# Optimization experiments

Hardware: AMD Instinct MI355X
Metric: run time of the kernel (lower is better)

Reference implementation:

```python
import jax, jax.numpy as jnp
import numpy as np

T = 16384       # video length (frames)
C = 7           # out_features = d_model = num surgical phases
F_DIM = 2048    # mstcn_f_dim (spatial feature dim)
LEN_Q = 30      # sliding window length
N_HEADS = 4
D_K = 64        # attn_dim = min(64, mstcn_f_maps=64)
D_FF = 64       # d_ff = mstcn_f_maps


def setup_inputs() -> dict:
    key = jax.random.key(0)
    ks = jax.random.split(key, 10)
    w = lambda i, shape: jax.random.normal(ks[i], shape, jnp.float32) * 0.05
    return {
        "x": jax.random.normal(ks[0], (1, C, T), jnp.float32),
        "long_feature": jax.random.normal(ks[1], (1, T, F_DIM), jnp.float32),
        "W_fc": w(2, (C, F_DIM)),              # nn.Linear(mstcn_f_dim, out_features, bias=False)
        "W_q": w(3, (N_HEADS * D_K, C)),
        "W_k": w(4, (N_HEADS * D_K, C)),
        "W_v": w(5, (N_HEADS * D_K, C)),
        "W_o": w(6, (C, N_HEADS * D_K)),
        "ln1_g": jnp.ones((C,), jnp.float32),
        "ln1_b": jnp.zeros((C,), jnp.float32),
        "W_ff1": w(7, (D_FF, C)),
        "W_ff2": w(8, (C, D_FF)),
        "ln2_g": jnp.ones((C,), jnp.float32),
        "ln2_b": jnp.zeros((C,), jnp.float32),
    }


def layer_norm(x, g, b, eps=1e-5):
    mu = x.mean(-1, keepdims=True)
    var = ((x - mu) ** 2).mean(-1, keepdims=True)
    return (x - mu) * jax.lax.rsqrt(var + eps) * g + b


def reference(x, long_feature, W_fc, W_q, W_k, W_v, W_o, ln1_g, ln1_b, W_ff1, W_ff2, ln2_g, ln2_b):
    # --- vectorized sliding-window (replaces the Python loop of zeros/cat/stack) ---
    feats = x[0].T                                            # (T, C)
    padded = jnp.concatenate([jnp.zeros((LEN_Q - 1, C), feats.dtype), feats], axis=0)
    idx = jnp.arange(T)[:, None] + jnp.arange(LEN_Q)[None, :]  # window ends at frame i
    inputs = padded[idx]                                       # (T, LEN_Q, C)

    # --- spatial embedding: feas = tanh(fc(long_feature)).transpose(0,1) ---
    feas = jnp.tanh(long_feature[0] @ W_fc.T)[:, None, :]      # (T, 1, C)

    # --- decoder layer: cross MHA(query=feas, kv=inputs) + residual + LN ---
    q = (feas @ W_q.T).reshape(T, 1, N_HEADS, D_K).transpose(0, 2, 1, 3)       # (T,H,1,Dk)
    k = (inputs @ W_k.T).reshape(T, LEN_Q, N_HEADS, D_K).transpose(0, 2, 1, 3)  # (T,H,Lq,Dk)
    v = (inputs @ W_v.T).reshape(T, LEN_Q, N_HEADS, D_K).transpose(0, 2, 1, 3)  # (T,H,Lq,Dk)
    scores = jnp.einsum('thqd,thkd->thqk', q, k) / np.float32(np.sqrt(D_K))
    attn = jax.nn.softmax(scores, axis=-1)
    ctx = jnp.einsum('thqk,thkd->thqd', attn, v)
    ctx = ctx.transpose(0, 2, 1, 3).reshape(T, 1, N_HEADS * D_K)
    out = layer_norm(ctx @ W_o.T + feas, ln1_g, ln1_b)         # (T, 1, C)

    # --- position-wise FFN + residual + LN ---
    ff = jax.nn.relu(out @ W_ff1.T) @ W_ff2.T
    out = layer_norm(ff + out, ln2_g, ln2_b)
    return out[:, 0]                                           # (T, C) per-frame logits
```

## Files before the change

kernel.cpp:

```cpp
#include <hip/hip_runtime.h>
#include <math.h>

#define T_FRAMES 16384
#define FDIM 2048
#define LQ 30
#define FPB 16

__global__ __launch_bounds__(448) void setup_kernel(
    const float* __restrict__ Wq, const float* __restrict__ Wk,
    const float* __restrict__ Wv, const float* __restrict__ Wo,
    float* __restrict__ AM) {
  const int e = threadIdx.x;
  if (e >= 392) return;
  const int which = e / 196;
  const int r = e % 196;
  const int h = r / 49;
  const int rr = r % 49;
  const int c = rr / 7;
  const int c2 = rr % 7;
  float s = 0.0f;
  if (which == 0) {
    for (int d = 0; d < 64; ++d)
      s = fmaf(Wq[(h * 64 + d) * 7 + c], Wk[(h * 64 + d) * 7 + c2], s);
  } else {
    for (int d = 0; d < 64; ++d)
      s = fmaf(Wo[c * 256 + h * 64 + d], Wv[(h * 64 + d) * 7 + c2], s);
  }
  AM[e] = s;
}

__global__ __launch_bounds__(256) void fused_kernel(
    const float* __restrict__ lf,
    const float* __restrict__ Wfc,
    const float* __restrict__ x,
    const float* __restrict__ AM,
    const float* __restrict__ W1,
    const float* __restrict__ W2,
    const float* __restrict__ ln1g, const float* __restrict__ ln1b,
    const float* __restrict__ ln2g, const float* __restrict__ ln2b,
    float* __restrict__ out) {
  __shared__ float feas_s[FPB][7];
  __shared__ float AM_s[392];
  __shared__ float ft[(FPB + LQ - 1) * 7];
  __shared__ float hpart[FPB][4][7];

  const int tid = threadIdx.x;
  const int lane = tid & 63;
  const int wave = tid >> 6;
  const int t0 = blockIdx.x * FPB;

  for (int i = tid; i < 392; i += 256) AM_s[i] = AM[i];
  for (int i = tid; i < (FPB + LQ - 1) * 7; i += 256) {
    const int row = i / 7, c = i % 7;
    const int s = t0 - (LQ - 1) + row;
    ft[i] = (s >= 0) ? x[c * T_FRAMES + s] : 0.0f;
  }

  const int tf = t0 + wave * 4;
  const float* lfp = lf + (size_t)tf * FDIM;
  float acc[4][7];
#pragma unroll
  for (int fr = 0; fr < 4; ++fr)
#pragma unroll
    for (int c = 0; c < 7; ++c) acc[fr][c] = 0.0f;

  for (int chunk = 0; chunk < 8; ++chunk) {
    const int f = chunk * 256 + lane * 4;
    const float4 a0 = *(const float4*)(lfp + 0 * FDIM + f);
    const float4 a1 = *(const float4*)(lfp + 1 * FDIM + f);
    const float4 a2 = *(const float4*)(lfp + 2 * FDIM + f);
    const float4 a3 = *(const float4*)(lfp + 3 * FDIM + f);
#pragma unroll
    for (int c = 0; c < 7; ++c) {
      const float4 w = *(const float4*)(Wfc + c * FDIM + f);
      acc[0][c] = fmaf(a0.x, w.x, fmaf(a0.y, w.y, fmaf(a0.z, w.z, fmaf(a0.w, w.w, acc[0][c]))));
      acc[1][c] = fmaf(a1.x, w.x, fmaf(a1.y, w.y, fmaf(a1.z, w.z, fmaf(a1.w, w.w, acc[1][c]))));
      acc[2][c] = fmaf(a2.x, w.x, fmaf(a2.y, w.y, fmaf(a2.z, w.z, fmaf(a2.w, w.w, acc[2][c]))));
      acc[3][c] = fmaf(a3.x, w.x, fmaf(a3.y, w.y, fmaf(a3.z, w.z, fmaf(a3.w, w.w, acc[3][c]))));
    }
  }

#pragma unroll
  for (int fr = 0; fr < 4; ++fr) {
#pragma unroll
    for (int c = 0; c < 7; ++c) {
      float v = acc[fr][c];
      for (int off = 32; off > 0; off >>= 1) v += __shfl_down(v, off, 64);
      if (lane == 0) feas_s[wave * 4 + fr][c] = tanhf(v);
    }
  }
  __syncthreads();

  if (tid < FPB * 4) {
    const int f = tid >> 2;
    const int h = tid & 3;
    float fe[7];
#pragma unroll
    for (int c = 0; c < 7; ++c) fe[c] = feas_s[f][c];

    const float* Ah = AM_s + h * 49;
    const float* Mh = AM_s + 196 + h * 49;
    float qk[7];
#pragma unroll
    for (int c2 = 0; c2 < 7; ++c2) {
      float s = 0.0f;
#pragma unroll
      for (int c = 0; c < 7; ++c) s = fmaf(fe[c], Ah[c * 7 + c2], s);
      qk[c2] = s * 0.125f;
    }
    const float* frow = &ft[f * 7];
    float sc[LQ];
    float m = -1e30f;
#pragma unroll
    for (int j = 0; j < LQ; ++j) {
      const float* r = frow + j * 7;
      float s = 0.0f;
#pragma unroll
      for (int c2 = 0; c2 < 7; ++c2) s = fmaf(qk[c2], r[c2], s);
      sc[j] = s;
      m = fmaxf(m, s);
    }
    float sum = 0.0f;
    float wsum[7] = {0, 0, 0, 0, 0, 0, 0};
#pragma unroll
    for (int j = 0; j < LQ; ++j) {
      const float p = __expf(sc[j] - m);
      sum += p;
      const float* r = frow + j * 7;
#pragma unroll
      for (int c2 = 0; c2 < 7; ++c2) wsum[c2] = fmaf(p, r[c2], wsum[c2]);
    }
    const float inv = 1.0f / sum;
#pragma unroll
    for (int c = 0; c < 7; ++c) {
      float s = 0.0f;
#pragma unroll
      for (int c2 = 0; c2 < 7; ++c2) s = fmaf(Mh[c * 7 + c2], wsum[c2], s);
      hpart[f][h][c] = s * inv;
    }
  }
  __syncthreads();

  if (tid < FPB) {
    const int f = tid;
    float v[7];
#pragma unroll
    for (int c = 0; c < 7; ++c)
      v[c] = feas_s[f][c] + hpart[f][0][c] + hpart[f][1][c] + hpart[f][2][c] + hpart[f][3][c];

    float mu = 0.0f;
#pragma unroll
    for (int c = 0; c < 7; ++c) mu += v[c];
    mu *= (1.0f / 7.0f);
    float var = 0.0f;
#pragma unroll
    for (int c = 0; c < 7; ++c) { const float d = v[c] - mu; var = fmaf(d, d, var); }
    var *= (1.0f / 7.0f);
    float rs = rsqrtf(var + 1e-5f);
    float o1[7];
#pragma unroll
    for (int c = 0; c < 7; ++c) o1[c] = (v[c] - mu) * rs * ln1g[c] + ln1b[c];

    float ff[7] = {0, 0, 0, 0, 0, 0, 0};
    for (int k = 0; k < 64; ++k) {
      float hk = 0.0f;
#pragma unroll
      for (int c = 0; c < 7; ++c) hk = fmaf(W1[k * 7 + c], o1[c], hk);
      hk = fmaxf(hk, 0.0f);
#pragma unroll
      for (int c = 0; c < 7; ++c) ff[c] = fmaf(W2[c * 64 + k], hk, ff[c]);
    }

#pragma unroll
    for (int c = 0; c < 7; ++c) v[c] = ff[c] + o1[c];
    mu = 0.0f;
#pragma unroll
    for (int c = 0; c < 7; ++c) mu += v[c];
    mu *= (1.0f / 7.0f);
    var = 0.0f;
#pragma unroll
    for (int c = 0; c < 7; ++c) { const float d = v[c] - mu; var = fmaf(d, d, var); }
    var *= (1.0f / 7.0f);
    rs = rsqrtf(var + 1e-5f);
    const int t = t0 + f;
#pragma unroll
    for (int c = 0; c < 7; ++c)
      out[(size_t)t * 7 + c] = (v[c] - mu) * rs * ln2g[c] + ln2b[c];
  }
}

extern "C" void kernel_launch(void* const* d_in, const int* in_sizes, int n_in,
                              void* d_out, int out_size, void* d_ws, size_t ws_size,
                              hipStream_t stream) {
  const float* x    = (const float*)d_in[0];
  const float* lf   = (const float*)d_in[1];
  const float* Wfc  = (const float*)d_in[2];
  const float* Wq   = (const float*)d_in[3];
  const float* Wk   = (const float*)d_in[4];
  const float* Wv   = (const float*)d_in[5];
  const float* Wo   = (const float*)d_in[6];
  const float* ln1g = (const float*)d_in[7];
  const float* ln1b = (const float*)d_in[8];
  const float* W1   = (const float*)d_in[9];
  const float* W2   = (const float*)d_in[10];
  const float* ln2g = (const float*)d_in[11];
  const float* ln2b = (const float*)d_in[12];
  float* out = (float*)d_out;

  float* AM = (float*)d_ws;

  setup_kernel<<<1, 448, 0, stream>>>(Wq, Wk, Wv, Wo, AM);
  fused_kernel<<<T_FRAMES / FPB, 256, 0, stream>>>(
      lf, Wfc, x, AM, W1, W2, ln1g, ln1b, ln2g, ln2b, out);
}
```

Baseline: 254.0 us.

## Split fused kernel into streaming feature GEMV and wide attention kernel

Separates the long_feature projection into its own kernel, with 8 frames per block and all sixteen float4 loads per thread issued before any math, to raise memory-level parallelism on the dominant 128 MB stream. The attention, LayerNorm and FFN stage moves to a second kernel handling 64 frames per block, so all 256 threads do attention instead of 64. The intermediate feas values are staged through the output buffer, which is safe because each block reads only its own frames before overwriting them. This adds an extra launch and a global round-trip for the small feas tensor.

```diff
diff --git a/kernel.cpp b/kernel.cpp
--- a/kernel.cpp
+++ b/kernel.cpp
@@ -4,7 +4,6 @@
 #define T_FRAMES 16384
 #define FDIM 2048
 #define LQ 30
-#define FPB 16
 
 __global__ __launch_bounds__(448) void setup_kernel(
     const float* __restrict__ Wq, const float* __restrict__ Wk,
@@ -29,69 +28,84 @@
   AM[e] = s;
 }
 
-__global__ __launch_bounds__(256) void fused_kernel(
+#define FPB_A 8
+
+__global__ __launch_bounds__(256) void feas_kernel(
     const float* __restrict__ lf,
     const float* __restrict__ Wfc,
+    float* __restrict__ feas) {
+  const int tid = threadIdx.x;
+  const int lane = tid & 63;
+  const int wave = tid >> 6;
+  const int t0 = blockIdx.x * FPB_A + wave * 2;
+  const float* lfp = lf + (size_t)t0 * FDIM + lane * 4;
+
+  float4 a0[8], a1[8];
+#pragma unroll
+  for (int ch = 0; ch < 8; ++ch) a0[ch] = *(const float4*)(lfp + ch * 256);
+#pragma unroll
+  for (int ch = 0; ch < 8; ++ch) a1[ch] = *(const float4*)(lfp + FDIM + ch * 256);
+
+  float acc0[7] = {0, 0, 0, 0, 0, 0, 0};
+  float acc1[7] = {0, 0, 0, 0, 0, 0, 0};
+#pragma unroll
+  for (int ch = 0; ch < 8; ++ch) {
+#pragma unroll
+    for (int c = 0; c < 7; ++c) {
+      const float4 w = *(const float4*)(Wfc + c * FDIM + ch * 256 + lane * 4);
+      acc0[c] = fmaf(a0[ch].x, w.x, fmaf(a0[ch].y, w.y,
+                fmaf(a0[ch].z, w.z, fmaf(a0[ch].w, w.w, acc0[c]))));
+      acc1[c] = fmaf(a1[ch].x, w.x, fmaf(a1[ch].y, w.y,
+                fmaf(a1[ch].z, w.z, fmaf(a1[ch].w, w.w, acc1[c]))));
+    }
+  }
+
+#pragma unroll
+  for (int c = 0; c < 7; ++c) {
+    float v0 = acc0[c];
+    float v1 = acc1[c];
+#pragma unroll
+    for (int off = 32; off > 0; off >>= 1) {
+      v0 += __shfl_down(v0, off, 64);
+      v1 += __shfl_down(v1, off, 64);
+    }
+    if (lane == 0) {
+      feas[(size_t)t0 * 7 + c]       = tanhf(v0);
+      feas[(size_t)(t0 + 1) * 7 + c] = tanhf(v1);
+    }
+  }
+}
+
+#define BF 64
+
+__global__ __launch_bounds__(256) void attn_kernel(
     const float* __restrict__ x,
+    const float* __restrict__ feas_g,
     const float* __restrict__ AM,
     const float* __restrict__ W1,
     const float* __restrict__ W2,
     const float* __restrict__ ln1g, const float* __restrict__ ln1b,
     const float* __restrict__ ln2g, const float* __restrict__ ln2b,
     float* __restrict__ out) {
-  __shared__ float feas_s[FPB][7];
   __shared__ float AM_s[392];
-  __shared__ float ft[(FPB + LQ - 1) * 7];
-  __shared__ float hpart[FPB][4][7];
+  __shared__ float ft[(BF + LQ - 1) * 7];
+  __shared__ float feas_s[BF][7];
+  __shared__ float hpart[BF][4][7];
 
   const int tid = threadIdx.x;
-  const int lane = tid & 63;
-  const int wave = tid >> 6;
-  const int t0 = blockIdx.x * FPB;
+  const int t0 = blockIdx.x * BF;
 
   for (int i = tid; i < 392; i += 256) AM_s[i] = AM[i];
-  for (int i = tid; i < (FPB + LQ - 1) * 7; i += 256) {
+  for (int i = tid; i < (BF + LQ - 1) * 7; i += 256) {
     const int row = i / 7, c = i % 7;
     const int s = t0 - (LQ - 1) + row;
     ft[i] = (s >= 0) ? x[c * T_FRAMES + s] : 0.0f;
   }
-
-  const int tf = t0 + wave * 4;
-  const float* lfp = lf + (size_t)tf * FDIM;
-  float acc[4][7];
-#pragma unroll
-  for (int fr = 0; fr < 4; ++fr)
-#pragma unroll
-    for (int c = 0; c < 7; ++c) acc[fr][c] = 0.0f;
-
-  for (int chunk = 0; chunk < 8; ++chunk) {
-    const int f = chunk * 256 + lane * 4;
-    const float4 a0 = *(const float4*)(lfp + 0 * FDIM + f);
-    const float4 a1 = *(const float4*)(lfp + 1 * FDIM + f);
-    const float4 a2 = *(const float4*)(lfp + 2 * FDIM + f);
-    const float4 a3 = *(const float4*)(lfp + 3 * FDIM + f);
-#pragma unroll
-    for (int c = 0; c < 7; ++c) {
-      const float4 w = *(const float4*)(Wfc + c * FDIM + f);
-      acc[0][c] = fmaf(a0.x, w.x, fmaf(a0.y, w.y, fmaf(a0.z, w.z, fmaf(a0.w, w.w, acc[0][c]))));
-      acc[1][c] = fmaf(a1.x, w.x, fmaf(a1.y, w.y, fmaf(a1.z, w.z, fmaf(a1.w, w.w, acc[1][c]))));
-      acc[2][c] = fmaf(a2.x, w.x, fmaf(a2.y, w.y, fmaf(a2.z, w.z, fmaf(a2.w, w.w, acc[2][c]))));
-      acc[3][c] = fmaf(a3.x, w.x, fmaf(a3.y, w.y, fmaf(a3.z, w.z, fmaf(a3.w, w.w, acc[3][c]))));
-    }
-  }
-
-#pragma unroll
-  for (int fr = 0; fr < 4; ++fr) {
-#pragma unroll
-    for (int c = 0; c < 7; ++c) {
-      float v = acc[fr][c];
-      for (int off = 32; off > 0; off >>= 1) v += __shfl_down(v, off, 64);
-      if (lane == 0) feas_s[wave * 4 + fr][c] = tanhf(v);
-    }
-  }
+  for (int i = tid; i < BF * 7; i += 256)
+    feas_s[i / 7][i % 7] = feas_g[(size_t)t0 * 7 + i];
   __syncthreads();
 
-  if (tid < FPB * 4) {
+  {
     const int f = tid >> 2;
     const int h = tid & 3;
     float fe[7];
@@ -141,7 +155,7 @@
   }
   __syncthreads();
 
-  if (tid < FPB) {
+  if (tid < BF) {
     const int f = tid;
     float v[7];
 #pragma unroll
@@ -210,6 +224,7 @@
   float* AM = (float*)d_ws;
 
   setup_kernel<<<1, 448, 0, stream>>>(Wq, Wk, Wv, Wo, AM);
-  fused_kernel<<<T_FRAMES / FPB, 256, 0, stream>>>(
-      lf, Wfc, x, AM, W1, W2, ln1g, ln1b, ln2g, ln2b, out);
-}
+  feas_kernel<<<T_FRAMES / FPB_A, 256, 0, stream>>>(lf, Wfc, out);
+  attn_kernel<<<T_FRAMES / BF, 256, 0, stream>>>(
+      x, out, AM, W1, W2, ln1g, ln1b, ln2g, ln2b, out);
+}
```

New measurement: 277.3 us. 1.09x slower.
